# Kernel optimization log

Measured on AMD Instinct MI355X. Metric: run time of the kernel, lower is better.

## Reference

```python
import jax, jax.numpy as jnp
import numpy as np

KH, KW = 3, 3  # window_size[1], window_size[2]
SH, SW = 1, 1  # strides
FILTERS = 64


def _extract_patches(x, kh, kw, sh, sw):
    # TF tf.image.extract_patches ordering: depth = (row, col, channel), channel fastest.
    B, H, W, C = x.shape
    Ho = (H - kh) // sh + 1
    Wo = (W - kw) // sw + 1
    # stack kh*kw shifted views -> (B, Ho, Wo, kh*kw, C)
    views = [x[:, i:i + (Ho - 1) * sh + 1:sh, j:j + (Wo - 1) * sw + 1:sw, :]
             for i in range(kh) for j in range(kw)]
    patches = jnp.stack(views, axis=3)
    return patches.reshape(B, Ho, Wo, kh * kw * C)


def setup_inputs() -> dict:
    key = jax.random.key(0)
    k1, k2 = jax.random.split(key)
    B, H, W, C = 8, 32, 32, 32
    K = KH * KW * C  # 288
    x = jax.random.normal(k1, (B, H, W, C), dtype=jnp.float32)
    w = jax.random.normal(k2, (1, 1, 1, K, FILTERS), dtype=jnp.float32) * 0.05
    bias = jnp.zeros((FILTERS,), dtype=jnp.float32)
    return {"x": x, "w": w, "bias": bias}


def reference(x, w, bias):
    # patches: (B, Ho, Wo, K)
    patches = _extract_patches(x, KH, KW, SH, SW)
    # broadcast add: (B, Ho, Wo, K, F)
    s = patches[..., None] + w
    # tropical max-plus minus min-plus over the patch axis, plus bias
    return jnp.max(s, axis=3) - jnp.min(s, axis=3) + bias
```

## Files before the change

kernel.cpp:

```cpp
#include <hip/hip_runtime.h>
#include <math.h>


#define TPB 512
#define PIX 2

__device__ __forceinline__ float fmax3(float a, float b, float c) {
    return fmaxf(fmaxf(a, b), c);
}
__device__ __forceinline__ float fmin3(float a, float b, float c) {
    return fminf(fminf(a, b), c);
}

__global__ __launch_bounds__(TPB) void trop_kernel(
    const float* __restrict__ x,
    const float* __restrict__ w,
    const float* __restrict__ bias,
    float* __restrict__ out)
{
    extern __shared__ float wlds[];

    const int tid  = threadIdx.x;
    const int lane = tid & 63;
    const int wv   = tid >> 6;

    const int pix0 = blockIdx.x * (8 * PIX) + wv * PIX;

    {
        const float4* src = (const float4*)w;
        float4* dst = (float4*)wlds;
#pragma unroll
        for (int i = 0; i < 9; ++i) dst[tid + i * 512] = src[tid + i * 512];
    }

    int xoffp[PIX];
#pragma unroll
    for (int p = 0; p < PIX; ++p) {
        const int pid = pix0 + p;
        const int wo = pid % 30;
        const int t  = pid / 30;
        const int ho = t % 30;
        const int b  = t / 30;
        xoffp[p] = __builtin_amdgcn_readfirstlane((((b * 32 + ho) * 32) + wo) * 32);
    }

    float amax[PIX], amin[PIX];
#pragma unroll
    for (int p = 0; p < PIX; ++p) { amax[p] = -INFINITY; amin[p] = INFINITY; }

    __syncthreads();

#pragma unroll
    for (int tap = 0; tap < 9; ++tap) {
        const int dy = tap / 3;
        const int dx = tap % 3;
        const int xoff = (dy * 32 + dx) * 32;
        const float* wl = wlds + tap * 2048;
#pragma unroll
        for (int c = 0; c < 32; c += 4) {
            const float w0 = wl[(c + 0) * 64 + lane];
            const float w1 = wl[(c + 1) * 64 + lane];
            const float w2 = wl[(c + 2) * 64 + lane];
            const float w3 = wl[(c + 3) * 64 + lane];
#pragma unroll
            for (int p = 0; p < PIX; ++p) {
                const float* xb = x + xoffp[p] + xoff;
                const float s0 = xb[c + 0] + w0;
                const float s1 = xb[c + 1] + w1;
                const float s2 = xb[c + 2] + w2;
                const float s3 = xb[c + 3] + w3;
                amax[p] = fmax3(amax[p], fmax3(s0, s1, s2), s3);
                amin[p] = fmin3(amin[p], fmin3(s0, s1, s2), s3);
            }
        }
    }

    const float bv = bias[lane];
#pragma unroll
    for (int p = 0; p < PIX; ++p)
        out[(pix0 + p) * 64 + lane] = amax[p] - amin[p] + bv;
}

extern "C" void kernel_launch(void* const* d_in, const int* in_sizes, int n_in,
                              void* d_out, int out_size, void* d_ws, size_t ws_size,
                              hipStream_t stream) {
    const float* x    = (const float*)d_in[0];
    const float* w    = (const float*)d_in[1];
    const float* bias = (const float*)d_in[2];
    float* out = (float*)d_out;

    static int attr_done = 0;
    if (!attr_done) {
        (void)hipFuncSetAttribute((const void*)trop_kernel,
                                  hipFuncAttributeMaxDynamicSharedMemorySize,
                                  73728);
        attr_done = 1;
    }

    trop_kernel<<<dim3(450), dim3(TPB), 73728, stream>>>(x, w, bias, out);
}
```

Measured before the change: 68.04 us.

## Transpose weights in LDS with padded stride and use float4 loads

```diff
diff --git a/kernel.cpp b/kernel.cpp
--- a/kernel.cpp
+++ b/kernel.cpp
@@ -4,6 +4,7 @@
 
 #define TPB 512
 #define PIX 2
+#define WSTRIDE 292
 
 __device__ __forceinline__ float fmax3(float a, float b, float c) {
     return fmaxf(fmaxf(a, b), c);
@@ -12,7 +13,7 @@
     return fminf(fminf(a, b), c);
 }
 
-__global__ __launch_bounds__(TPB) void trop_kernel(
+__global__ __launch_bounds__(TPB, 4) void trop_kernel(
     const float* __restrict__ x,
     const float* __restrict__ w,
     const float* __restrict__ bias,
@@ -28,12 +29,20 @@
 
     {
         const float4* src = (const float4*)w;
-        float4* dst = (float4*)wlds;
 #pragma unroll
-        for (int i = 0; i < 9; ++i) dst[tid + i * 512] = src[tid + i * 512];
+        for (int i = 0; i < 9; ++i) {
+            const int e4 = tid + i * 512;
+            const float4 v = src[e4];
+            const int k = e4 >> 4;
+            const int f = (e4 & 15) * 4;
+            wlds[(f + 0) * WSTRIDE + k] = v.x;
+            wlds[(f + 1) * WSTRIDE + k] = v.y;
+            wlds[(f + 2) * WSTRIDE + k] = v.z;
+            wlds[(f + 3) * WSTRIDE + k] = v.w;
+        }
     }
 
-    int xoffp[PIX];
+    const float* xp[PIX];
 #pragma unroll
     for (int p = 0; p < PIX; ++p) {
         const int pid = pix0 + p;
@@ -41,7 +50,7 @@
         const int t  = pid / 30;
         const int ho = t % 30;
         const int b  = t / 30;
-        xoffp[p] = __builtin_amdgcn_readfirstlane((((b * 32 + ho) * 32) + wo) * 32);
+        xp[p] = x + (((b * 32 + ho) * 32) + wo) * 32;
     }
 
     float amax[PIX], amin[PIX];
@@ -50,25 +59,23 @@
 
     __syncthreads();
 
+    const float* wrow = wlds + lane * WSTRIDE;
+
 #pragma unroll
     for (int tap = 0; tap < 9; ++tap) {
         const int dy = tap / 3;
         const int dx = tap % 3;
         const int xoff = (dy * 32 + dx) * 32;
-        const float* wl = wlds + tap * 2048;
 #pragma unroll
         for (int c = 0; c < 32; c += 4) {
-            const float w0 = wl[(c + 0) * 64 + lane];
-            const float w1 = wl[(c + 1) * 64 + lane];
-            const float w2 = wl[(c + 2) * 64 + lane];
-            const float w3 = wl[(c + 3) * 64 + lane];
+            const float4 wv4 = *(const float4*)(wrow + tap * 32 + c);
 #pragma unroll
             for (int p = 0; p < PIX; ++p) {
-                const float* xb = x + xoffp[p] + xoff;
-                const float s0 = xb[c + 0] + w0;
-                const float s1 = xb[c + 1] + w1;
-                const float s2 = xb[c + 2] + w2;
-                const float s3 = xb[c + 3] + w3;
+                const float4 xv = *(const float4*)(xp[p] + xoff + c);
+                const float s0 = xv.x + wv4.x;
+                const float s1 = xv.y + wv4.y;
+                const float s2 = xv.z + wv4.z;
+                const float s3 = xv.w + wv4.w;
                 amax[p] = fmax3(amax[p], fmax3(s0, s1, s2), s3);
                 amin[p] = fmin3(amin[p], fmin3(s0, s1, s2), s3);
             }
@@ -93,9 +100,9 @@
     if (!attr_done) {
         (void)hipFuncSetAttribute((const void*)trop_kernel,
                                   hipFuncAttributeMaxDynamicSharedMemorySize,
-                                  73728);
+                                  74752);
         attr_done = 1;
     }
 
-    trop_kernel<<<dim3(450), dim3(TPB), 73728, stream>>>(x, w, bias, out);
+    trop_kernel<<<dim3(450), dim3(TPB), 74752, stream>>>(x, w, bias, out);
 }
```

Result: slower. 77.50 us (+13.9%).
